# Kernel optimization log

Measured on AMD Instinct MI355X. Metric: run time of the kernel, lower is better.

The kernel has to match this reference:

```python
import jax, jax.numpy as jnp
import numpy as np

D_MODEL = 1024
N_HEADS = 16
HEAD_DIM = D_MODEL // N_HEADS


def setup_inputs() -> dict:
    key = jax.random.key(0)
    k1, k2, k3 = jax.random.split(key, 3)
    x = jax.random.normal(k1, (4, 2048, D_MODEL), dtype=jnp.float32)
    # per-head qkv Linear (bias=False): torch weight [3*head_dim, d_model];
    # store transposed and stacked over heads: [H, d_model, 3*head_dim]
    w_qkv = jax.random.normal(k2, (N_HEADS, D_MODEL, 3 * HEAD_DIM), dtype=jnp.float32) * (1.0 / np.sqrt(D_MODEL))
    # output Linear (bias=False), stored transposed: [d_model, d_model]
    w_out = jax.random.normal(k3, (D_MODEL, D_MODEL), dtype=jnp.float32) * (1.0 / np.sqrt(D_MODEL))
    return {"x": x, "w_qkv": w_qkv, "w_out": w_out}


def reference(x, w_qkv, w_out):
    hd = HEAD_DIM
    # all heads' qkv in one contraction: [B, H, S, 3*hd]
    qkv = jnp.einsum("bsd,hde->bhse", x, w_qkv)
    q, k, v = qkv[..., :hd], qkv[..., hd:2 * hd], qkv[..., 2 * hd:]
    scale = 1.0 / hd  # NOTE: original scales by 1/dk, not 1/sqrt(dk)
    scores = jnp.einsum("bhqe,bhke->bhqk", q, k) * scale
    attn = jax.nn.softmax(scores, axis=-1)
    z = jnp.einsum("bhqk,bhke->bhqe", attn, v)  # [B, H, S, hd]
    # concat heads along feature dim (head order = list order)
    b, h, s, _ = z.shape
    z = jnp.transpose(z, (0, 2, 1, 3)).reshape(b, s, h * hd)
    return z @ w_out
```

## Files before the change

kernel.cpp:

```cpp
#include <hip/hip_runtime.h>
#include <hip/hip_bf16.h>

typedef unsigned short u16;
typedef __attribute__((ext_vector_type(4))) float f32x4;
typedef __attribute__((ext_vector_type(16))) float f32x16;
typedef __attribute__((ext_vector_type(8))) short s16x8;
typedef __attribute__((ext_vector_type(4))) unsigned short u16x4;

static __device__ __forceinline__ u16 f32_to_bf16(float f) {
    union { float f; unsigned u; } v; v.f = f;
    unsigned r = v.u + 0x7FFF + ((v.u >> 16) & 1);
    return (u16)(r >> 16);
}

static __device__ __forceinline__ unsigned cvt_pk_bf16(float lo, float hi) {
    unsigned r;
    asm("v_cvt_pk_bf16_f32 %0, %1, %2" : "=v"(r) : "v"(lo), "v"(hi));
    return r;
}

static __device__ __forceinline__ void pswap2(unsigned &a, unsigned &b) {
#if defined(__has_builtin) && __has_builtin(__builtin_amdgcn_permlane32_swap)
    auto r = __builtin_amdgcn_permlane32_swap(a, b, false, false);
    a = r[0]; b = r[1];
#else
    asm volatile("v_permlane32_swap_b32 %0, %1" : "+v"(a), "+v"(b));
#endif
}

static __device__ __forceinline__ float xhalf_sum(float x) {
    unsigned a = __float_as_uint(x), b = a;
    pswap2(a, b);
    return __uint_as_float(a) + __uint_as_float(b);
}

static __device__ __forceinline__ float fexp2(float x) {
#if defined(__has_builtin) && __has_builtin(__builtin_amdgcn_exp2f)
    return __builtin_amdgcn_exp2f(x);
#else
    return exp2f(x);
#endif
}

#define GLOAD_LDS16(gptr, lptr) \
    __builtin_amdgcn_global_load_lds((const __attribute__((address_space(1))) void*)(gptr), \
                                     (__attribute__((address_space(3))) void*)(lptr), 16, 0, 0)


__global__ void cvt_f32_bf16(const float* __restrict__ in, u16* __restrict__ out, int n) {
    int i = (blockIdx.x * 256 + threadIdx.x) * 4;
    if (i + 3 < n) {
        f32x4 v = *(const f32x4*)(in + i);
        u16x4 o;
        o.x = f32_to_bf16(v.x); o.y = f32_to_bf16(v.y);
        o.z = f32_to_bf16(v.z); o.w = f32_to_bf16(v.w);
        *(u16x4*)(out + i) = o;
    }
}

__global__ void cvt_wqkvT(const float* __restrict__ w, u16* __restrict__ wt) {
    int tid = blockIdx.x * 256 + threadIdx.x;
    int k = tid & 1023, n = tid >> 10;
    int h = n / 192, e = n - h * 192;
    wt[tid] = f32_to_bf16(w[(h * 1024 + k) * 192 + e]);
}

__global__ void cvt_woutT(const float* __restrict__ w, u16* __restrict__ wt) {
    int tid = blockIdx.x * 256 + threadIdx.x;
    int k = tid & 1023, n = tid >> 10;
    wt[tid] = f32_to_bf16(w[k * 1024 + n]);
}


template <int EPI>
__global__ __launch_bounds__(256, 2)
void gemm_bt(const u16* __restrict__ A, const u16* __restrict__ B,
             float* __restrict__ Cf, u16* __restrict__ Qb, u16* __restrict__ Kb,
             u16* __restrict__ Vt, int M, int N, int K) {
    __shared__ __align__(16) u16 lA[128 * 64];
    __shared__ __align__(16) u16 lB[128 * 64];

    const int t = threadIdx.x;
    const int lane = t & 63;
    const int wave = t >> 6;
    const int wr = wave >> 1, wc = wave & 1;
    const int l15 = lane & 15, g = lane >> 4;

    const int nwg = gridDim.x;
    const int cpx = nwg >> 3;
    const int orig = blockIdx.x;
    const int logical = (orig & 7) * cpx + (orig >> 3);

    const int nbx = N >> 7;
    const int bx = logical % nbx, by = logical / nbx;
    const int bm = by << 7, bn = bx << 7;

    f32x4 acc[4][4] = {};

    const int rA = t >> 3;
    const int cA = (t & 7) * 8;

    for (int kt = 0; kt < K; kt += 64) {
#pragma unroll
        for (int c = 0; c < 4; ++c) {
            int row = rA + 32 * c;
            GLOAD_LDS16(A + (size_t)(bm + row) * K + kt + cA, lA + row * 64 + cA);
        }
#pragma unroll
        for (int c = 0; c < 4; ++c) {
            int row = rA + 32 * c;
            GLOAD_LDS16(B + (size_t)(bn + row) * K + kt + cA, lB + row * 64 + cA);
        }
        __syncthreads();
#pragma unroll
        for (int kk = 0; kk < 2; ++kk) {
            s16x8 a[4], b[4];
#pragma unroll
            for (int i = 0; i < 4; ++i)
                a[i] = *(const s16x8*)(lA + (wr * 64 + i * 16 + l15) * 64 + kk * 32 + g * 8);
#pragma unroll
            for (int j = 0; j < 4; ++j)
                b[j] = *(const s16x8*)(lB + (wc * 64 + j * 16 + l15) * 64 + kk * 32 + g * 8);
#pragma unroll
            for (int i = 0; i < 4; ++i)
#pragma unroll
                for (int j = 0; j < 4; ++j)
                    acc[i][j] = __builtin_amdgcn_mfma_f32_16x16x32_bf16(a[i], b[j], acc[i][j], 0, 0, 0);
        }
        __syncthreads();
    }

    if constexpr (EPI == 0) {
#pragma unroll
        for (int i = 0; i < 4; ++i) {
            int row0 = bm + wr * 64 + i * 16 + g * 4;
#pragma unroll
            for (int j = 0; j < 4; ++j) {
                int col = bn + wc * 64 + j * 16 + l15;
#pragma unroll
                for (int r = 0; r < 4; ++r)
                    Cf[(size_t)(row0 + r) * N + col] = acc[i][j][r];
            }
        }
    } else {
        const float qscale = 0.022542110013890054f;
#pragma unroll
        for (int j = 0; j < 4; ++j) {
            int n = bn + wc * 64 + j * 16 + l15;
            int h = n / 192;
            int e = n - h * 192;
#pragma unroll
            for (int i = 0; i < 4; ++i) {
                int m0 = bm + wr * 64 + i * 16 + g * 4;
#pragma unroll
                for (int r = 0; r < 4; ++r) {
                    int m = m0 + r;
                    int b = m >> 11, s = m & 2047;
                    int bh = b * 16 + h;
                    float av = acc[i][j][r];
                    if (e < 64)       Qb[((size_t)bh * 2048 + s) * 64 + e] = f32_to_bf16(av * qscale);
                    else if (e < 128) Kb[((size_t)bh * 2048 + s) * 64 + (e - 64)] = f32_to_bf16(av);
                    else              Vt[((size_t)bh * 64 + (e - 128)) * 2048 + s] = f32_to_bf16(av);
                }
            }
        }
    }
}

__global__ __launch_bounds__(512, 4)
void attn32(const u16* __restrict__ Qb, const u16* __restrict__ Kb,
            const u16* __restrict__ Vt, u16* __restrict__ Zb) {
    __shared__ __align__(16) u16 lK[2][64 * 64];
    __shared__ __align__(16) u16 lV[2][64 * 64];
    __shared__ float lds_l[8][32];

    const int t = threadIdx.x;
    const int lane = t & 63;
    const int w = t >> 6;
    const int l31 = lane & 31, hi = lane >> 5;
    const int r7 = l31 & 7;

    const int orig = blockIdx.x;
    const int logical = (orig & 7) * 64 + (orig >> 3);
    const int bh = logical >> 3;
    const int qt = logical & 7;
    const int q0 = qt * 256 + w * 32;

    const u16* Kbh = Kb + (size_t)bh * 2048 * 64;
    const u16* Vbh = Vt + (size_t)bh * 64 * 2048;

    const int lr = lane >> 3;
    const int lc = (lane & 7) ^ lr;

    const u16* Qp = Qb + ((size_t)bh * 2048 + q0 + l31) * 64 + hi * 8;
    s16x8 qf[4];
#pragma unroll
    for (int kd = 0; kd < 4; ++kd) qf[kd] = *(const s16x8*)(Qp + kd * 16);

    f32x16 o0 = {}, o1 = {};
    float l = 0.f;

#define STAGE(buf, kvn) do { \
    int gr = w * 8 + lr; \
    GLOAD_LDS16(Kbh + (size_t)((kvn) + gr) * 64 + lc * 8, \
                &lK[buf][w * 512 + lane * 8]); \
    GLOAD_LDS16(Vbh + (size_t)gr * 2048 + (kvn) + lc * 8, \
                &lV[buf][w * 512 + lane * 8]); \
    } while (0)

    STAGE(0, 0);
    __syncthreads();

#pragma unroll 2
    for (int ti = 0; ti < 32; ++ti) {
        const int cur = ti & 1;
        const int kvn = ((ti + 1) & 31) * 64;

        STAGE(cur ^ 1, kvn);

        const u16* Kc = &lK[cur][0];
        f32x16 p0 = {}, p1 = {};
        __builtin_amdgcn_s_setprio(1);
#pragma unroll
        for (int kd = 0; kd < 4; ++kd) {
            int cs = ((hi + 2 * kd) ^ r7) * 8;
            s16x8 kf0 = *(const s16x8*)&Kc[l31 * 64 + cs];
            p0 = __builtin_amdgcn_mfma_f32_32x32x16_bf16(kf0, qf[kd], p0, 0, 0, 0);
            s16x8 kf1 = *(const s16x8*)&Kc[(l31 + 32) * 64 + cs];
            p1 = __builtin_amdgcn_mfma_f32_32x32x16_bf16(kf1, qf[kd], p1, 0, 0, 0);
        }
        __builtin_amdgcn_s_setprio(0);

        float rs = 0.f;
#pragma unroll
        for (int r = 0; r < 16; ++r) {
            p0[r] = fexp2(p0[r]); rs += p0[r];
            p1[r] = fexp2(p1[r]); rs += p1[r];
        }
        l += xhalf_sum(rs);

        union { unsigned u[8]; s16x8 v[2]; } pa0, pa1;
        {
            unsigned c0 = cvt_pk_bf16(p0[0],  p0[1]);
            unsigned c1 = cvt_pk_bf16(p0[2],  p0[3]);
            unsigned c2 = cvt_pk_bf16(p0[4],  p0[5]);
            unsigned c3 = cvt_pk_bf16(p0[6],  p0[7]);
            unsigned c4 = cvt_pk_bf16(p0[8],  p0[9]);
            unsigned c5 = cvt_pk_bf16(p0[10], p0[11]);
            unsigned c6 = cvt_pk_bf16(p0[12], p0[13]);
            unsigned c7 = cvt_pk_bf16(p0[14], p0[15]);
            pswap2(c0, c2); pswap2(c1, c3);
            pswap2(c4, c6); pswap2(c5, c7);
            pa0.u[0] = c0; pa0.u[1] = c1; pa0.u[2] = c2; pa0.u[3] = c3;
            pa0.u[4] = c4; pa0.u[5] = c5; pa0.u[6] = c6; pa0.u[7] = c7;
        }
        {
            unsigned c0 = cvt_pk_bf16(p1[0],  p1[1]);
            unsigned c1 = cvt_pk_bf16(p1[2],  p1[3]);
            unsigned c2 = cvt_pk_bf16(p1[4],  p1[5]);
            unsigned c3 = cvt_pk_bf16(p1[6],  p1[7]);
            unsigned c4 = cvt_pk_bf16(p1[8],  p1[9]);
            unsigned c5 = cvt_pk_bf16(p1[10], p1[11]);
            unsigned c6 = cvt_pk_bf16(p1[12], p1[13]);
            unsigned c7 = cvt_pk_bf16(p1[14], p1[15]);
            pswap2(c0, c2); pswap2(c1, c3);
            pswap2(c4, c6); pswap2(c5, c7);
            pa1.u[0] = c0; pa1.u[1] = c1; pa1.u[2] = c2; pa1.u[3] = c3;
            pa1.u[4] = c4; pa1.u[5] = c5; pa1.u[6] = c6; pa1.u[7] = c7;
        }

        const u16* Vc = &lV[cur][0];
        __builtin_amdgcn_s_setprio(1);
#pragma unroll
        for (int ks = 0; ks < 4; ++ks) {
            s16x8 pav = (ks < 2) ? pa0.v[ks & 1] : pa1.v[ks & 1];
            int cs = ((hi + 2 * ks) ^ r7) * 8;
            s16x8 vf0 = *(const s16x8*)&Vc[l31 * 64 + cs];
            o0 = __builtin_amdgcn_mfma_f32_32x32x16_bf16(pav, vf0, o0, 0, 0, 0);
            s16x8 vf1 = *(const s16x8*)&Vc[(l31 + 32) * 64 + cs];
            o1 = __builtin_amdgcn_mfma_f32_32x32x16_bf16(pav, vf1, o1, 0, 0, 0);
        }
        __builtin_amdgcn_s_setprio(0);

        __syncthreads();
    }
#undef STAGE

    if (lane < 32) lds_l[w][l31] = l;
    __syncthreads();

    const int b = bh >> 4, h = bh & 15;
#pragma unroll
    for (int r = 0; r < 16; ++r) {
        int qrow = (r & 3) + 8 * (r >> 2) + 4 * hi;
        float inv = 1.0f / lds_l[w][qrow];
        size_t rowbase = ((size_t)(b * 2048 + q0 + qrow)) * 1024 + h * 64 + l31;
        Zb[rowbase]      = f32_to_bf16(o0[r] * inv);
        Zb[rowbase + 32] = f32_to_bf16(o1[r] * inv);
    }
}


extern "C" void kernel_launch(void* const* d_in, const int* in_sizes, int n_in,
                              void* d_out, int out_size, void* d_ws, size_t ws_size,
                              hipStream_t stream) {
    const float* x     = (const float*)d_in[0];
    const float* w_qkv = (const float*)d_in[1];
    const float* w_out = (const float*)d_in[2];
    float* out = (float*)d_out;

    char* ws = (char*)d_ws;
    u16* xb  = (u16*)ws; ws += (size_t)8192 * 1024 * 2;
    u16* wqT = (u16*)ws; ws += (size_t)3072 * 1024 * 2;
    u16* woT = (u16*)ws; ws += (size_t)1024 * 1024 * 2;
    u16* Qb  = (u16*)ws; ws += (size_t)64 * 2048 * 64 * 2;
    u16* Kb  = (u16*)ws; ws += (size_t)64 * 2048 * 64 * 2;
    u16* Vt  = (u16*)ws; ws += (size_t)64 * 2048 * 64 * 2;
    u16* Zb  = (u16*)ws; ws += (size_t)8192 * 1024 * 2;

    cvt_f32_bf16<<<dim3(8192), dim3(256), 0, stream>>>(x, xb, 8192 * 1024);
    cvt_wqkvT<<<dim3(12288), dim3(256), 0, stream>>>(w_qkv, wqT);
    cvt_woutT<<<dim3(4096), dim3(256), 0, stream>>>(w_out, woT);

    gemm_bt<1><<<dim3(64 * 24), dim3(256), 0, stream>>>(xb, wqT, nullptr, Qb, Kb, Vt,
                                                        8192, 3072, 1024);
    attn32<<<dim3(512), dim3(512), 0, stream>>>(Qb, Kb, Vt, Zb);
    gemm_bt<0><<<dim3(64 * 8), dim3(256), 0, stream>>>(Zb, woT, out, nullptr, nullptr, nullptr,
                                                       8192, 1024, 1024);
}
```

Before: 216.4 us.

## Double-buffer GEMM LDS tiles with swizzle, vectorize epilogue stores, split softmax sums

The bf16 GEMM now uses a two-stage LDS buffer with K-tile 32, prefetching the next tile while computing the current one, and XOR-swizzles the LDS layout to avoid bank conflicts. It swaps the MFMA operand order so each lane holds 4 consecutive columns, which allows vectorized f32x4 and u16x4 stores for C, Q and K. Launch bounds are raised to 4 blocks per CU. In the attention kernel, the row-sum accumulation is split into four independent chains to shorten the dependency latency. The halved K-tile doubles the number of barriers, and the higher occupancy target may constrain registers.

New measurement: 210.6 us. -2.7%, faster.

```diff
diff --git a/kernel.cpp b/kernel.cpp
--- a/kernel.cpp
+++ b/kernel.cpp
@@ -73,12 +73,12 @@
 
 
 template <int EPI>
-__global__ __launch_bounds__(256, 2)
+__global__ __launch_bounds__(256, 4)
 void gemm_bt(const u16* __restrict__ A, const u16* __restrict__ B,
              float* __restrict__ Cf, u16* __restrict__ Qb, u16* __restrict__ Kb,
              u16* __restrict__ Vt, int M, int N, int K) {
-    __shared__ __align__(16) u16 lA[128 * 64];
-    __shared__ __align__(16) u16 lB[128 * 64];
+    __shared__ __align__(16) u16 lA[2][128 * 32];
+    __shared__ __align__(16) u16 lB[2][128 * 32];
 
     const int t = threadIdx.x;
     const int lane = t & 63;
@@ -97,70 +97,87 @@
 
     f32x4 acc[4][4] = {};
 
-    const int rA = t >> 3;
-    const int cA = (t & 7) * 8;
-
-    for (int kt = 0; kt < K; kt += 64) {
-#pragma unroll
-        for (int c = 0; c < 4; ++c) {
-            int row = rA + 32 * c;
-            GLOAD_LDS16(A + (size_t)(bm + row) * K + kt + cA, lA + row * 64 + cA);
-        }
-#pragma unroll
-        for (int c = 0; c < 4; ++c) {
-            int row = rA + 32 * c;
-            GLOAD_LDS16(B + (size_t)(bn + row) * K + kt + cA, lB + row * 64 + cA);
-        }
+    const int sr0 = t >> 2;
+    const int ss  = t & 3;
+
+    const u16* Abase = A + (size_t)bm * K;
+    const u16* Bbase = B + (size_t)bn * K;
+
+#define GSTAGE(buf, kt) do { \
+    _Pragma("unroll") \
+    for (int c = 0; c < 2; ++c) { \
+        int r = sr0 + 64 * c; \
+        int cl = ss ^ (r & 3); \
+        GLOAD_LDS16(Abase + (size_t)r * K + (kt) + cl * 8, &lA[buf][(r * 4 + ss) * 8]); \
+        GLOAD_LDS16(Bbase + (size_t)r * K + (kt) + cl * 8, &lB[buf][(r * 4 + ss) * 8]); \
+    } } while (0)
+
+    GSTAGE(0, 0);
+
+    const int NT = K >> 5;
+    for (int ti = 0; ti < NT; ++ti) {
         __syncthreads();
-#pragma unroll
-        for (int kk = 0; kk < 2; ++kk) {
-            s16x8 a[4], b[4];
-#pragma unroll
-            for (int i = 0; i < 4; ++i)
-                a[i] = *(const s16x8*)(lA + (wr * 64 + i * 16 + l15) * 64 + kk * 32 + g * 8);
+        if (ti + 1 < NT) GSTAGE((ti + 1) & 1, (ti + 1) << 5);
+
+        const u16* Ac = lA[ti & 1];
+        const u16* Bc = lB[ti & 1];
+        s16x8 a[4], b[4];
+#pragma unroll
+        for (int i = 0; i < 4; ++i) {
+            int r = wr * 64 + i * 16 + l15;
+            int sl = g ^ (r & 3);
+            a[i] = *(const s16x8*)&Ac[(r * 4 + sl) * 8];
+        }
+#pragma unroll
+        for (int j = 0; j < 4; ++j) {
+            int r = wc * 64 + j * 16 + l15;
+            int sl = g ^ (r & 3);
+            b[j] = *(const s16x8*)&Bc[(r * 4 + sl) * 8];
+        }
+#pragma unroll
+        for (int i = 0; i < 4; ++i)
 #pragma unroll
             for (int j = 0; j < 4; ++j)
-                b[j] = *(const s16x8*)(lB + (wc * 64 + j * 16 + l15) * 64 + kk * 32 + g * 8);
-#pragma unroll
-            for (int i = 0; i < 4; ++i)
-#pragma unroll
-                for (int j = 0; j < 4; ++j)
-                    acc[i][j] = __builtin_amdgcn_mfma_f32_16x16x32_bf16(a[i], b[j], acc[i][j], 0, 0, 0);
-        }
-        __syncthreads();
-    }
+                acc[i][j] = __builtin_amdgcn_mfma_f32_16x16x32_bf16(b[j], a[i], acc[i][j], 0, 0, 0);
+    }
+#undef GSTAGE
 
     if constexpr (EPI == 0) {
 #pragma unroll
         for (int i = 0; i < 4; ++i) {
-            int row0 = bm + wr * 64 + i * 16 + g * 4;
+            int m = bm + wr * 64 + i * 16 + l15;
 #pragma unroll
             for (int j = 0; j < 4; ++j) {
-                int col = bn + wc * 64 + j * 16 + l15;
-#pragma unroll
-                for (int r = 0; r < 4; ++r)
-                    Cf[(size_t)(row0 + r) * N + col] = acc[i][j][r];
+                int n0 = bn + wc * 64 + j * 16 + g * 4;
+                *(f32x4*)&Cf[(size_t)m * N + n0] = acc[i][j];
             }
         }
     } else {
         const float qscale = 0.022542110013890054f;
 #pragma unroll
         for (int j = 0; j < 4; ++j) {
-            int n = bn + wc * 64 + j * 16 + l15;
-            int h = n / 192;
-            int e = n - h * 192;
+            int n0 = bn + wc * 64 + j * 16 + g * 4;
+            int h = n0 / 192;
+            int e0 = n0 - h * 192;
 #pragma unroll
             for (int i = 0; i < 4; ++i) {
-                int m0 = bm + wr * 64 + i * 16 + g * 4;
-#pragma unroll
-                for (int r = 0; r < 4; ++r) {
-                    int m = m0 + r;
-                    int b = m >> 11, s = m & 2047;
-                    int bh = b * 16 + h;
-                    float av = acc[i][j][r];
-                    if (e < 64)       Qb[((size_t)bh * 2048 + s) * 64 + e] = f32_to_bf16(av * qscale);
-                    else if (e < 128) Kb[((size_t)bh * 2048 + s) * 64 + (e - 64)] = f32_to_bf16(av);
-                    else              Vt[((size_t)bh * 64 + (e - 128)) * 2048 + s] = f32_to_bf16(av);
+                int m = bm + wr * 64 + i * 16 + l15;
+                int bb = m >> 11, s = m & 2047;
+                int bh = bb * 16 + h;
+                if (e0 < 64) {
+                    u16x4 q;
+#pragma unroll
+                    for (int r = 0; r < 4; ++r) q[r] = f32_to_bf16(acc[i][j][r] * qscale);
+                    *(u16x4*)&Qb[((size_t)bh * 2048 + s) * 64 + e0] = q;
+                } else if (e0 < 128) {
+                    u16x4 kk;
+#pragma unroll
+                    for (int r = 0; r < 4; ++r) kk[r] = f32_to_bf16(acc[i][j][r]);
+                    *(u16x4*)&Kb[((size_t)bh * 2048 + s) * 64 + (e0 - 64)] = kk;
+                } else {
+#pragma unroll
+                    for (int r = 0; r < 4; ++r)
+                        Vt[((size_t)bh * 64 + (e0 - 128 + r)) * 2048 + s] = f32_to_bf16(acc[i][j][r]);
                 }
             }
         }
@@ -231,13 +248,19 @@
         }
         __builtin_amdgcn_s_setprio(0);
 
-        float rs = 0.f;
-#pragma unroll
-        for (int r = 0; r < 16; ++r) {
-            p0[r] = fexp2(p0[r]); rs += p0[r];
-            p1[r] = fexp2(p1[r]); rs += p1[r];
-        }
-        l += xhalf_sum(rs);
+        float rs0 = 0.f, rs1 = 0.f, rs2 = 0.f, rs3 = 0.f;
+#pragma unroll
+        for (int r = 0; r < 16; r += 4) {
+            p0[r]     = fexp2(p0[r]);     rs0 += p0[r];
+            p0[r + 1] = fexp2(p0[r + 1]); rs1 += p0[r + 1];
+            p0[r + 2] = fexp2(p0[r + 2]); rs2 += p0[r + 2];
+            p0[r + 3] = fexp2(p0[r + 3]); rs3 += p0[r + 3];
+            p1[r]     = fexp2(p1[r]);     rs0 += p1[r];
+            p1[r + 1] = fexp2(p1[r + 1]); rs1 += p1[r + 1];
+            p1[r + 2] = fexp2(p1[r + 2]); rs2 += p1[r + 2];
+            p1[r + 3] = fexp2(p1[r + 3]); rs3 += p1[r + 3];
+        }
+        l += xhalf_sum((rs0 + rs1) + (rs2 + rs3));
 
         union { unsigned u[8]; s16x8 v[2]; } pa0, pa1;
         {
```
